# Performance work log

Measured on AMD Instinct MI355X. Metric: run time of the kernel, lower is better.

## Reference

```python
import jax, jax.numpy as jnp
import numpy as np

M_FACTORS = [8, 8, 8, 8]
N_FACTORS = [8, 8, 8, 8]
RANK = 8
E = 8
B = 8
SEQ = 512
M_IN = int(np.prod(M_FACTORS))   # 4096
N_OUT = int(np.prod(N_FACTORS))  # 4096


def setup_inputs() -> dict:
    key = jax.random.key(0)
    k1, k2, k3, k4, k5 = jax.random.split(key, 5)
    X = jax.random.normal(k1, (B, SEQ, M_IN), dtype=jnp.float32)
    gates = jax.random.uniform(k2, (B, E), dtype=jnp.float32)
    # TT cores: [E, r_i, factor, r_{i+1}]; boundary ranks are 1.
    core_first = jax.random.normal(k3, (E, 1, M_FACTORS[0], RANK), dtype=jnp.float32)
    cores_mid = jax.random.normal(k4, (6, E, RANK, 8, RANK), dtype=jnp.float32)
    core_last = jax.random.normal(k5, (E, RANK, N_FACTORS[-1], 1), dtype=jnp.float32)
    return {"X": X, "gates": gates, "core_first": core_first,
            "cores_mid": cores_mid, "core_last": core_last}


def _tt_forward(X, gates, core_first, cores_mid, core_last):
    b, s, _ = X.shape
    # View X as [B, 1, seq, m_k-1, ..., m_0] (m factors reversed), rank dim = 1.
    tt = X.reshape((b, s) + tuple(M_FACTORS[::-1]))[:, None]
    cores = [core_first] + [cores_mid[i] for i in range(cores_mid.shape[0])] + [core_last]
    num_m = len(M_FACTORS)
    # Input-factor contractions: 'b r ... m, b r m p -> b p ...'
    for i in range(num_m):
        merged = jnp.einsum('be,ermp->brmp', gates, cores[i])  # [B, r, m_f, p]
        tt = jnp.einsum('br...m,brmp->bp...', tt, merged)
    # Output-factor expansions: 'b r ..., b r n p -> b p ... n'
    for i in range(len(N_FACTORS)):
        merged = jnp.einsum('be,ernp->brnp', gates, cores[num_m + i])  # [B, r, n_f, p]
        tt = jnp.einsum('br...,brnp->bp...n', tt, merged)
    return tt.reshape(b, s, -1)  # [B, seq, prod(n_factors)]


def reference(X, gates, core_first, cores_mid, core_last):
    return _tt_forward(X, gates, core_first, cores_mid, core_last)
```

## Files before the change

### kernel.cpp

```cpp
#include <hip/hip_runtime.h>

typedef float f32x4 __attribute__((ext_vector_type(4)));

#define GLOBAL_AS __attribute__((address_space(1)))
#define SHARED_AS __attribute__((address_space(3)))


__global__ __launch_bounds__(256) void k_compose(
    const float* __restrict__ gates,
    const float* __restrict__ core_first,
    const float* __restrict__ cores_mid,
    const float* __restrict__ core_last,
    float* __restrict__ KinT,
    float* __restrict__ Kout)
{
  const int part = blockIdx.x;
  const int b    = blockIdx.y;
  const int z    = blockIdx.z;
  const int t    = threadIdx.x;

  __shared__ float g[8];
  __shared__ float mg[1600];
  __shared__ __align__(16) float S1[512];
  __shared__ __align__(16) float S2[128 * 9];

  if (t < 8) g[t] = gates[b*8 + t];
  __syncthreads();

  if (z < 4) {
    for (int idx = t; idx < 1600; idx += 256) {
      float acc = 0.f;
      if (idx < 64) {
        #pragma unroll
        for (int e = 0; e < 8; ++e) acc += g[e] * core_first[e*64 + idx];
      } else {
        const int i = (idx - 64) >> 9;
        const int w2 = (idx - 64) & 511;
        #pragma unroll
        for (int e = 0; e < 8; ++e) acc += g[e] * cores_mid[(i*8 + e)*512 + w2];
      }
      mg[idx] = acc;
    }
    __syncthreads();

    #pragma unroll
    for (int i = 0; i < 2; ++i) {
      const int idx = i*256 + t;
      const int mm = idx >> 3, p2 = idx & 7;
      const int m1 = mm >> 3, m0 = mm & 7;
      float acc = 0.f;
      #pragma unroll
      for (int p1 = 0; p1 < 8; ++p1)
        acc += mg[m0*8 + p1] * mg[64 + p1*64 + m1*8 + p2];
      S1[idx] = acc;
    }
    __syncthreads();

    #pragma unroll
    for (int i = 0; i < 4; ++i) {
      const int idx = i*256 + t;
      const int rl = idx >> 3, p3 = idx & 7;
      const int m2 = 2*z + (rl >> 6), mm = rl & 63;
      float acc = 0.f;
      #pragma unroll
      for (int p2 = 0; p2 < 8; ++p2)
        acc += S1[mm*8 + p2] * mg[576 + p2*64 + m2*8 + p3];
      S2[rl*9 + p3] = acc;
    }
    __syncthreads();

    float* kb = KinT + b*32768;
    #pragma unroll
    for (int i = 0; i < 4; ++i) {
      const int idx = i*256 + t;
      const int rl = idx >> 3, p4 = idx & 7;
      float acc = 0.f;
      #pragma unroll
      for (int p3 = 0; p3 < 8; ++p3)
        acc += S2[rl*9 + p3] * mg[1088 + p3*64 + part*8 + p4];
      kb[p4*4096 + part*512 + z*128 + rl] = acc;
    }
  } else {
    const int zz = z - 4;
    for (int idx = t; idx < 1600; idx += 256) {
      float acc = 0.f;
      if (idx < 1536) {
        const int i = 3 + (idx >> 9);
        const int w2 = idx & 511;
        #pragma unroll
        for (int e = 0; e < 8; ++e) acc += g[e] * cores_mid[(i*8 + e)*512 + w2];
      } else {
        const int w2 = idx - 1536;
        #pragma unroll
        for (int e = 0; e < 8; ++e) acc += g[e] * core_last[e*64 + w2];
      }
      mg[idx] = acc;
    }
    __syncthreads();

    #pragma unroll
    for (int i = 0; i < 2; ++i) {
      const int id = i*256 + t;
      const int p6 = id >> 6, n2 = (id >> 3) & 7, n3 = id & 7;
      float acc = 0.f;
      #pragma unroll
      for (int p7 = 0; p7 < 8; ++p7)
        acc += mg[1024 + p6*64 + n2*8 + p7] * mg[1536 + p7*8 + n3];
      S1[id] = acc;
    }
    __syncthreads();

    #pragma unroll
    for (int i = 0; i < 4; ++i) {
      const int idx = i*256 + t;
      const int p5 = idx >> 7, jl = idx & 127;
      const int n1 = 2*zz + (jl >> 6), nn = jl & 63;
      float acc = 0.f;
      #pragma unroll
      for (int p6 = 0; p6 < 8; ++p6)
        acc += mg[512 + p5*64 + n1*8 + p6] * S1[p6*64 + nn];
      S2[p5*128 + jl] = acc;
    }
    __syncthreads();

    float* ob = Kout + b*32768 + part*512 + zz*128;
    #pragma unroll
    for (int i = 0; i < 4; ++i) {
      const int idx = i*256 + t;
      const int jl = idx >> 3, p4 = idx & 7;
      float acc = 0.f;
      #pragma unroll
      for (int p5 = 0; p5 < 8; ++p5)
        acc += mg[p4*64 + part*8 + p5] * S2[p5*128 + jl];
      ob[p4*4096 + jl] = acc;
    }
  }
}

__global__ __launch_bounds__(256) void k_fused(
    const float* __restrict__ X,
    const float* __restrict__ KinT,
    const float* __restrict__ Kout,
    float* __restrict__ Out)
{
  const int stile = blockIdx.x;
  const int b     = blockIdx.y;
  const int t     = threadIdx.x;
  const int lane  = t & 63;
  const int w     = t >> 6;

  __shared__ __align__(16) float xs[4][8 * 256];
  __shared__ __align__(16) float ks[4][8 * 256];
  __shared__ float vs[8 * 8];

  const int s0 = stile * 8;
  const float* xsrc = X    + ((size_t)(b*512 + s0)) * 4096;
  const float* ksrc = KinT + (size_t)b*32768;

#define STAGE(c, u) do {                                                       \
    const int off_ = (c)*256 + lane*4;                                         \
    __builtin_amdgcn_global_load_lds(                                          \
        (const GLOBAL_AS void*)(xsrc + (size_t)(w)*4096 + off_),               \
        (SHARED_AS void*)&xs[u][(w)*256], 16, 0, 0);                           \
    __builtin_amdgcn_global_load_lds(                                          \
        (const GLOBAL_AS void*)(xsrc + (size_t)(w + 4)*4096 + off_),           \
        (SHARED_AS void*)&xs[u][(w + 4)*256], 16, 0, 0);                       \
    __builtin_amdgcn_global_load_lds(                                          \
        (const GLOBAL_AS void*)(ksrc + (size_t)(w)*4096 + off_),               \
        (SHARED_AS void*)&ks[u][(w)*256], 16, 0, 0);                           \
    __builtin_amdgcn_global_load_lds(                                          \
        (const GLOBAL_AS void*)(ksrc + (size_t)(w + 4)*4096 + off_),           \
        (SHARED_AS void*)&ks[u][(w + 4)*256], 16, 0, 0);                       \
  } while (0)

  const int r0 = w*2, r1 = w*2 + 1;

  f32x4 acc0[8], acc1[8];
  #pragma unroll
  for (int p = 0; p < 8; ++p) { acc0[p] = (f32x4)0.f; acc1[p] = (f32x4)0.f; }

  STAGE(0, 0);
  STAGE(1, 1);
  STAGE(2, 2);

  #pragma unroll
  for (int c = 0; c < 16; ++c) {
    if (c <= 13)      asm volatile("s_waitcnt vmcnt(8)" ::: "memory");
    else if (c == 14) asm volatile("s_waitcnt vmcnt(4)" ::: "memory");
    else              asm volatile("s_waitcnt vmcnt(0)" ::: "memory");
    __builtin_amdgcn_s_barrier();
    if (c + 3 < 16) STAGE(c + 3, (c + 3) & 3);

    const int u = c & 3;
    const f32x4 x0 = *(const f32x4*)&xs[u][r0*256 + lane*4];
    const f32x4 x1 = *(const f32x4*)&xs[u][r1*256 + lane*4];
    #pragma unroll
    for (int p = 0; p < 8; ++p) {
      const f32x4 k = *(const f32x4*)&ks[u][p*256 + lane*4];
      acc0[p] += x0 * k;
      acc1[p] += x1 * k;
    }
  }
#undef STAGE

  #pragma unroll
  for (int p = 0; p < 8; ++p) {
    float s0v = acc0[p].x + acc0[p].y + acc0[p].z + acc0[p].w;
    float s1v = acc1[p].x + acc1[p].y + acc1[p].z + acc1[p].w;
    #pragma unroll
    for (int d = 1; d < 64; d <<= 1) {
      s0v += __shfl_xor(s0v, d);
      s1v += __shfl_xor(s1v, d);
    }
    if (lane == 0) {
      vs[r0*8 + p] = s0v;
      vs[r1*8 + p] = s1v;
    }
  }
  __syncthreads();

  float4 vA[8], vB[8];
  #pragma unroll
  for (int s = 0; s < 8; ++s) {
    vA[s] = *(const float4*)(vs + s*8);
    vB[s] = *(const float4*)(vs + s*8 + 4);
  }

  const float* kob = Kout + (size_t)b*32768 + t*4;
  float*       ob  = Out + ((size_t)(b*512 + s0))*4096 + t*4;

  #pragma unroll
  for (int nc = 0; nc < 4; ++nc) {
    float4 kr[8];
    #pragma unroll
    for (int p = 0; p < 8; ++p)
      kr[p] = *(const float4*)(kob + p*4096 + nc*1024);
    #pragma unroll
    for (int s = 0; s < 8; ++s) {
      f32x4 o;
      o.x = vA[s].x*kr[0].x + vA[s].y*kr[1].x + vA[s].z*kr[2].x + vA[s].w*kr[3].x
          + vB[s].x*kr[4].x + vB[s].y*kr[5].x + vB[s].z*kr[6].x + vB[s].w*kr[7].x;
      o.y = vA[s].x*kr[0].y + vA[s].y*kr[1].y + vA[s].z*kr[2].y + vA[s].w*kr[3].y
          + vB[s].x*kr[4].y + vB[s].y*kr[5].y + vB[s].z*kr[6].y + vB[s].w*kr[7].y;
      o.z = vA[s].x*kr[0].z + vA[s].y*kr[1].z + vA[s].z*kr[2].z + vA[s].w*kr[3].z
          + vB[s].x*kr[4].z + vB[s].y*kr[5].z + vB[s].z*kr[6].z + vB[s].w*kr[7].z;
      o.w = vA[s].x*kr[0].w + vA[s].y*kr[1].w + vA[s].z*kr[2].w + vA[s].w*kr[3].w
          + vB[s].x*kr[4].w + vB[s].y*kr[5].w + vB[s].z*kr[6].w + vB[s].w*kr[7].w;
      __builtin_nontemporal_store(o, (f32x4*)(ob + (size_t)s*4096 + nc*1024));
    }
  }
}

extern "C" void kernel_launch(void* const* d_in, const int* in_sizes, int n_in,
                              void* d_out, int out_size, void* d_ws, size_t ws_size,
                              hipStream_t stream) {
  const float* X     = (const float*)d_in[0];
  const float* gates = (const float*)d_in[1];
  const float* cf    = (const float*)d_in[2];
  const float* cm    = (const float*)d_in[3];
  const float* cl    = (const float*)d_in[4];
  float* out = (float*)d_out;

  float* ws   = (float*)d_ws;
  float* KinT = ws;
  float* Kout = ws + 262144;

  k_compose<<<dim3(8, 8, 8), 256, 0, stream>>>(gates, cf, cm, cl, KinT, Kout);
  k_fused  <<<dim3(64, 8),   256, 0, stream>>>(X, KinT, Kout, out);
}
```

Measured before the change: 159.8 us.

## Replace LDS-staged pipeline with direct global loads, one sequence row per wave

The fused kernel drops the async global-to-LDS multi-buffered staging of X and KinT. Each wave now streams one sequence row straight from global memory into registers, and the tile shrinks from 8 to 4 rows per block, doubling the grid to 128x8 blocks. This removes the LDS traffic and barriers and raises block count and occupancy. In exchange, each KinT element is now read from global/L2 once per row rather than shared across 8 rows, so the main loop leans on cache bandwidth and has no explicit prefetch.

```diff
diff --git a/kernel.cpp b/kernel.cpp
--- a/kernel.cpp
+++ b/kernel.cpp
@@ -1,9 +1,6 @@
 #include <hip/hip_runtime.h>
 
 typedef float f32x4 __attribute__((ext_vector_type(4)));
-
-#define GLOBAL_AS __attribute__((address_space(1)))
-#define SHARED_AS __attribute__((address_space(3)))
 
 
 __global__ __launch_bounds__(256) void k_compose(
@@ -149,85 +146,51 @@
   const int lane  = t & 63;
   const int w     = t >> 6;
 
-  __shared__ __align__(16) float xs[4][8 * 256];
-  __shared__ __align__(16) float ks[4][8 * 256];
-  __shared__ float vs[8 * 8];
-
-  const int s0 = stile * 8;
-  const float* xsrc = X    + ((size_t)(b*512 + s0)) * 4096;
-  const float* ksrc = KinT + (size_t)b*32768;
-
-#define STAGE(c, u) do {                                                       \
-    const int off_ = (c)*256 + lane*4;                                         \
-    __builtin_amdgcn_global_load_lds(                                          \
-        (const GLOBAL_AS void*)(xsrc + (size_t)(w)*4096 + off_),               \
-        (SHARED_AS void*)&xs[u][(w)*256], 16, 0, 0);                           \
-    __builtin_amdgcn_global_load_lds(                                          \
-        (const GLOBAL_AS void*)(xsrc + (size_t)(w + 4)*4096 + off_),           \
-        (SHARED_AS void*)&xs[u][(w + 4)*256], 16, 0, 0);                       \
-    __builtin_amdgcn_global_load_lds(                                          \
-        (const GLOBAL_AS void*)(ksrc + (size_t)(w)*4096 + off_),               \
-        (SHARED_AS void*)&ks[u][(w)*256], 16, 0, 0);                           \
-    __builtin_amdgcn_global_load_lds(                                          \
-        (const GLOBAL_AS void*)(ksrc + (size_t)(w + 4)*4096 + off_),           \
-        (SHARED_AS void*)&ks[u][(w + 4)*256], 16, 0, 0);                       \
-  } while (0)
-
-  const int r0 = w*2, r1 = w*2 + 1;
-
-  f32x4 acc0[8], acc1[8];
-  #pragma unroll
-  for (int p = 0; p < 8; ++p) { acc0[p] = (f32x4)0.f; acc1[p] = (f32x4)0.f; }
-
-  STAGE(0, 0);
-  STAGE(1, 1);
-  STAGE(2, 2);
-
-  #pragma unroll
-  for (int c = 0; c < 16; ++c) {
-    if (c <= 13)      asm volatile("s_waitcnt vmcnt(8)" ::: "memory");
-    else if (c == 14) asm volatile("s_waitcnt vmcnt(4)" ::: "memory");
-    else              asm volatile("s_waitcnt vmcnt(0)" ::: "memory");
-    __builtin_amdgcn_s_barrier();
-    if (c + 3 < 16) STAGE(c + 3, (c + 3) & 3);
-
-    const int u = c & 3;
-    const f32x4 x0 = *(const f32x4*)&xs[u][r0*256 + lane*4];
-    const f32x4 x1 = *(const f32x4*)&xs[u][r1*256 + lane*4];
-    #pragma unroll
-    for (int p = 0; p < 8; ++p) {
-      const f32x4 k = *(const f32x4*)&ks[u][p*256 + lane*4];
-      acc0[p] += x0 * k;
-      acc1[p] += x1 * k;
-    }
-  }
-#undef STAGE
+  __shared__ float vs[4 * 8];
+
+  const int s = stile*4 + w;
+  const float* xrow = X    + ((size_t)(b*512 + s))*4096 + lane*4;
+  const float* kb   = KinT + (size_t)b*32768 + lane*4;
+
+  f32x4 acc[8];
+  #pragma unroll
+  for (int p = 0; p < 8; ++p) acc[p] = (f32x4)0.f;
+
+  #pragma unroll
+  for (int j = 0; j < 16; ++j) {
+    const f32x4 x  = *(const f32x4*)(xrow + j*256);
+    const f32x4 k0 = *(const f32x4*)(kb + 0*4096 + j*256);
+    const f32x4 k1 = *(const f32x4*)(kb + 1*4096 + j*256);
+    const f32x4 k2 = *(const f32x4*)(kb + 2*4096 + j*256);
+    const f32x4 k3 = *(const f32x4*)(kb + 3*4096 + j*256);
+    const f32x4 k4 = *(const f32x4*)(kb + 4*4096 + j*256);
+    const f32x4 k5 = *(const f32x4*)(kb + 5*4096 + j*256);
+    const f32x4 k6 = *(const f32x4*)(kb + 6*4096 + j*256);
+    const f32x4 k7 = *(const f32x4*)(kb + 7*4096 + j*256);
+    acc[0] += x * k0;  acc[1] += x * k1;
+    acc[2] += x * k2;  acc[3] += x * k3;
+    acc[4] += x * k4;  acc[5] += x * k5;
+    acc[6] += x * k6;  acc[7] += x * k7;
+  }
 
   #pragma unroll
   for (int p = 0; p < 8; ++p) {
-    float s0v = acc0[p].x + acc0[p].y + acc0[p].z + acc0[p].w;
-    float s1v = acc1[p].x + acc1[p].y + acc1[p].z + acc1[p].w;
-    #pragma unroll
-    for (int d = 1; d < 64; d <<= 1) {
-      s0v += __shfl_xor(s0v, d);
-      s1v += __shfl_xor(s1v, d);
-    }
-    if (lane == 0) {
-      vs[r0*8 + p] = s0v;
-      vs[r1*8 + p] = s1v;
-    }
+    float v = acc[p].x + acc[p].y + acc[p].z + acc[p].w;
+    #pragma unroll
+    for (int d = 1; d < 64; d <<= 1) v += __shfl_xor(v, d);
+    if (lane == 0) vs[w*8 + p] = v;
   }
   __syncthreads();
 
-  float4 vA[8], vB[8];
-  #pragma unroll
-  for (int s = 0; s < 8; ++s) {
-    vA[s] = *(const float4*)(vs + s*8);
-    vB[s] = *(const float4*)(vs + s*8 + 4);
+  float4 vA[4], vB[4];
+  #pragma unroll
+  for (int sl = 0; sl < 4; ++sl) {
+    vA[sl] = *(const float4*)(vs + sl*8);
+    vB[sl] = *(const float4*)(vs + sl*8 + 4);
   }
 
   const float* kob = Kout + (size_t)b*32768 + t*4;
-  float*       ob  = Out + ((size_t)(b*512 + s0))*4096 + t*4;
+  float*       ob  = Out + ((size_t)(b*512 + stile*4))*4096 + t*4;
 
   #pragma unroll
   for (int nc = 0; nc < 4; ++nc) {
@@ -236,17 +199,17 @@
     for (int p = 0; p < 8; ++p)
       kr[p] = *(const float4*)(kob + p*4096 + nc*1024);
     #pragma unroll
-    for (int s = 0; s < 8; ++s) {
+    for (int sl = 0; sl < 4; ++sl) {
       f32x4 o;
-      o.x = vA[s].x*kr[0].x + vA[s].y*kr[1].x + vA[s].z*kr[2].x + vA[s].w*kr[3].x
-          + vB[s].x*kr[4].x + vB[s].y*kr[5].x + vB[s].z*kr[6].x + vB[s].w*kr[7].x;
-      o.y = vA[s].x*kr[0].y + vA[s].y*kr[1].y + vA[s].z*kr[2].y + vA[s].w*kr[3].y
-          + vB[s].x*kr[4].y + vB[s].y*kr[5].y + vB[s].z*kr[6].y + vB[s].w*kr[7].y;
-      o.z = vA[s].x*kr[0].z + vA[s].y*kr[1].z + vA[s].z*kr[2].z + vA[s].w*kr[3].z
-          + vB[s].x*kr[4].z + vB[s].y*kr[5].z + vB[s].z*kr[6].z + vB[s].w*kr[7].z;
-      o.w = vA[s].x*kr[0].w + vA[s].y*kr[1].w + vA[s].z*kr[2].w + vA[s].w*kr[3].w
-          + vB[s].x*kr[4].w + vB[s].y*kr[5].w + vB[s].z*kr[6].w + vB[s].w*kr[7].w;
-      __builtin_nontemporal_store(o, (f32x4*)(ob + (size_t)s*4096 + nc*1024));
+      o.x = vA[sl].x*kr[0].x + vA[sl].y*kr[1].x + vA[sl].z*kr[2].x + vA[sl].w*kr[3].x
+          + vB[sl].x*kr[4].x + vB[sl].y*kr[5].x + vB[sl].z*kr[6].x + vB[sl].w*kr[7].x;
+      o.y = vA[sl].x*kr[0].y + vA[sl].y*kr[1].y + vA[sl].z*kr[2].y + vA[sl].w*kr[3].y
+          + vB[sl].x*kr[4].y + vB[sl].y*kr[5].y + vB[sl].z*kr[6].y + vB[sl].w*kr[7].y;
+      o.z = vA[sl].x*kr[0].z + vA[sl].y*kr[1].z + vA[sl].z*kr[2].z + vA[sl].w*kr[3].z
+          + vB[sl].x*kr[4].z + vB[sl].y*kr[5].z + vB[sl].z*kr[6].z + vB[sl].w*kr[7].z;
+      o.w = vA[sl].x*kr[0].w + vA[sl].y*kr[1].w + vA[sl].z*kr[2].w + vA[sl].w*kr[3].w
+          + vB[sl].x*kr[4].w + vB[sl].y*kr[5].w + vB[sl].z*kr[6].w + vB[sl].w*kr[7].w;
+      __builtin_nontemporal_store(o, (f32x4*)(ob + (size_t)sl*4096 + nc*1024));
     }
   }
 }
@@ -266,5 +229,5 @@
   float* Kout = ws + 262144;
 
   k_compose<<<dim3(8, 8, 8), 256, 0, stream>>>(gates, cf, cm, cl, KinT, Kout);
-  k_fused  <<<dim3(64, 8),   256, 0, stream>>>(X, KinT, Kout, out);
+  k_fused  <<<dim3(128, 8),  256, 0, stream>>>(X, KinT, Kout, out);
 }
```

After: 155.4 us. 1.03x faster.
